# Kernel optimization log

Measured on AMD Instinct MI355X. Metric: run time of the kernel, lower is better.

## Reference

```python
import jax, jax.numpy as jnp
import numpy as np
import math

D_MODEL = 512
N_HEADS = 8
K_NEIGHBORS = 30
B, S = 4, 2048
N_VARIATES = 8
EPS = 1e-5


def layer_norm(x, g, b):
    m = jnp.mean(x, axis=-1, keepdims=True)
    v = jnp.mean(jnp.square(x - m), axis=-1, keepdims=True)
    return (x - m) * jax.lax.rsqrt(v + EPS) * g + b


def mha(x, mask, w_in, b_in, w_out, b_out):
    # x: [B,S,D]; mask: [B,S,S] bool, True = blocked (same for every head)
    Bb, Ss, D = x.shape
    H, dh = N_HEADS, D // N_HEADS
    qkv = x @ w_in.T + b_in                      # [B,S,3D]
    q, k, v = jnp.split(qkv, 3, axis=-1)
    q = q.reshape(Bb, Ss, H, dh).transpose(0, 2, 1, 3)
    k = k.reshape(Bb, Ss, H, dh).transpose(0, 2, 1, 3)
    v = v.reshape(Bb, Ss, H, dh).transpose(0, 2, 1, 3)
    scores = jnp.einsum('bhqd,bhkd->bhqk', q, k) / math.sqrt(dh)
    scores = jnp.where(mask[:, None, :, :], -jnp.inf, scores)
    attn = jax.nn.softmax(scores, axis=-1)
    o = jnp.einsum('bhqk,bhkd->bhqd', attn, v)
    o = o.transpose(0, 2, 1, 3).reshape(Bb, Ss, D)
    return o @ w_out.T + b_out


def build_masks(variates, times, valid_mask):
    Bb, Ss = variates.shape
    eye = jnp.eye(Ss, dtype=bool)
    same_var = variates[:, :, None] == variates[:, None, :]      # [B,S,S]
    valid_2d = valid_mask[:, :, None] & valid_mask[:, None, :]
    intra_mask = ~(same_var & valid_2d)                          # True = blocked
    blocked_i = jnp.any(jnp.all(intra_mask, axis=-1))
    intra_mask = intra_mask & ~(blocked_i & eye)                 # unblock diagonal if any row fully blocked

    diff_var = ~same_var
    time_dist = jnp.abs(times[:, :, None] - times[:, None, :])
    time_dist = jnp.where(~valid_2d | ~diff_var, jnp.inf, time_dist)
    k = min(K_NEIGHBORS, Ss)
    _, topk_idx = jax.lax.top_k(-time_dist, k)                   # k smallest distances
    b_idx = jnp.arange(Bb)[:, None, None]
    r_idx = jnp.arange(Ss)[None, :, None]
    knn_mask = jnp.zeros((Bb, Ss, Ss), dtype=bool).at[b_idx, r_idx, topk_idx].set(True)
    knn_mask = knn_mask & valid_2d
    inter_mask = ~knn_mask
    blocked_e = jnp.any(jnp.all(inter_mask, axis=-1))
    inter_mask = inter_mask & ~(blocked_e & eye)
    return intra_mask, inter_mask


def setup_inputs() -> dict:
    key = jax.random.key(0)
    ks = jax.random.split(key, 12)
    D = D_MODEL
    s = 0.02
    inp = {
        'x': jax.random.normal(ks[0], (B, S, D), dtype=jnp.float32),
        'variates': jax.random.randint(ks[1], (B, S), 0, N_VARIATES),
        'times': jax.random.uniform(ks[2], (B, S), dtype=jnp.float32),
        'valid_mask': jnp.ones((B, S), dtype=bool),
        'in_w1': jax.random.normal(ks[3], (3 * D, D), dtype=jnp.float32) * s,
        'in_b1': jnp.zeros((3 * D,), dtype=jnp.float32),
        'out_w1': jax.random.normal(ks[4], (D, D), dtype=jnp.float32) * s,
        'out_b1': jnp.zeros((D,), dtype=jnp.float32),
        'ln_g1': jnp.ones((D,), dtype=jnp.float32),
        'ln_b1': jnp.zeros((D,), dtype=jnp.float32),
        'in_w2': jax.random.normal(ks[5], (3 * D, D), dtype=jnp.float32) * s,
        'in_b2': jnp.zeros((3 * D,), dtype=jnp.float32),
        'out_w2': jax.random.normal(ks[6], (D, D), dtype=jnp.float32) * s,
        'out_b2': jnp.zeros((D,), dtype=jnp.float32),
        'ln_g2': jnp.ones((D,), dtype=jnp.float32),
        'ln_b2': jnp.zeros((D,), dtype=jnp.float32),
    }
    return inp


def reference(x, variates, times, valid_mask,
              in_w1, in_b1, out_w1, out_b1, ln_g1, ln_b1,
              in_w2, in_b2, out_w2, out_b2, ln_g2, ln_b2):
    intra_mask, inter_mask = build_masks(variates, times, valid_mask)
    a1 = mha(x, intra_mask, in_w1, in_b1, out_w1, out_b1)
    x = layer_norm(x + a1, ln_g1, ln_b1)
    a2 = mha(x, inter_mask, in_w2, in_b2, out_w2, out_b2)
    x = layer_norm(x + a2, ln_g2, ln_b2)
    return x
```

## Files before the change

### kernel.cpp

```cpp
#include <hip/hip_runtime.h>


#define S_LEN 2048
#define BATCH 4
#define DM    512
#define NH    8
#define DH    64
#define KNN_K 30
#define NVAR  8
#define NTOK  (BATCH * S_LEN)
#define QKVD  (3 * DM)
#define PADCAP 2560
#define MAXTILE 40

typedef float f32x4 __attribute__((ext_vector_type(4)));
typedef short s16x8 __attribute__((ext_vector_type(8)));
typedef short s16x4 __attribute__((ext_vector_type(4)));

__device__ __forceinline__ float bf2f(short u) {
  return __uint_as_float(((unsigned)(unsigned short)u) << 16);
}
__device__ __forceinline__ short f2bf(float f) {
  unsigned x = __float_as_uint(f);
  return (short)((x + 0x7fffu + ((x >> 16) & 1u)) >> 16);
}

#define C_N0 (NTOK * DM / 4)
#define C_N1 (QKVD * DM / 4)
#define C_N2 (DM * DM / 4)
#define C_B1 (C_N0 + C_N1)
#define C_B2 (C_B1 + C_N2)
#define C_B3 (C_B2 + C_N1)
#define C_B4 (C_B3 + C_N2)
#define PREP_GRID (2 * BATCH + C_B4 / 1024)

__global__ __launch_bounds__(1024) void prep_cast(
    const int* __restrict__ variates, const float* __restrict__ times,
    int* __restrict__ gcnt, int* __restrict__ pgoff, int* __restrict__ porig,
    int* __restrict__ tileV, int* __restrict__ tileQ0, int* __restrict__ ntile,
    float* __restrict__ flistT, int* __restrict__ flistI, int* __restrict__ flenG,
    int* __restrict__ sortI,
    const float* __restrict__ s0, const float* __restrict__ s1,
    const float* __restrict__ s2, const float* __restrict__ s3,
    const float* __restrict__ s4, short* __restrict__ d0,
    short* __restrict__ d1, short* __restrict__ d2,
    short* __restrict__ d3, short* __restrict__ d4) {
  int blk = blockIdx.x;
  int tid = threadIdx.x;

  if (blk < BATCH) {
    int b = blk;
    __shared__ unsigned hcnt[2048];
    __shared__ int boff[2049];
    __shared__ float bt[S_LEN];
    __shared__ int bp2[S_LEN];
    __shared__ unsigned wsum[16];
    __shared__ unsigned woff[16];

    hcnt[tid] = 0; hcnt[tid + 1024] = 0;
    float t0 = times[b * S_LEN + tid];
    float t1 = times[b * S_LEN + tid + 1024];
    int p0 = (variates[b * S_LEN + tid] << 12) | tid;
    int p1 = (variates[b * S_LEN + tid + 1024] << 12) | (tid + 1024);
    int k0 = (int)(t0 * 2048.0f); k0 = k0 < 0 ? 0 : (k0 > 2047 ? 2047 : k0);
    int k1 = (int)(t1 * 2048.0f); k1 = k1 < 0 ? 0 : (k1 > 2047 ? 2047 : k1);
    __syncthreads();
    atomicAdd(&hcnt[k0], 1u);
    atomicAdd(&hcnt[k1], 1u);
    __syncthreads();
    int wv = tid >> 6, lane = tid & 63;
    int base = wv * 128 + lane * 2;
    unsigned c0 = hcnt[base], c1 = hcnt[base + 1];
    unsigned s = c0 + c1;
    unsigned inc = s;
#pragma unroll
    for (int o2 = 1; o2 < 64; o2 <<= 1) {
      unsigned tt = __shfl_up(inc, o2);
      if (lane >= o2) inc += tt;
    }
    if (lane == 63) wsum[wv] = inc;
    __syncthreads();
    if (tid == 0) {
      unsigned a = 0;
      for (int w2 = 0; w2 < 16; ++w2) { woff[w2] = a; a += wsum[w2]; }
    }
    __syncthreads();
    unsigned e0 = woff[wv] + (inc - s);
    unsigned e1 = e0 + c0;
    boff[base] = (int)e0; boff[base + 1] = (int)e1;
    hcnt[base] = e0; hcnt[base + 1] = e1;
    if (tid == 0) boff[2048] = S_LEN;
    __syncthreads();
    unsigned q0 = atomicAdd(&hcnt[k0], 1u);
    bt[q0] = t0; bp2[q0] = p0;
    unsigned q1 = atomicAdd(&hcnt[k1], 1u);
    bt[q1] = t1; bp2[q1] = p1;
    __syncthreads();
#pragma unroll
    for (int bk = 0; bk < 2; ++bk) {
      int k = tid + bk * 1024;
      int s2 = boff[k], e2 = boff[k + 1];
      for (int i = s2 + 1; i < e2; ++i) {
        float tv = bt[i]; int pv = bp2[i];
        int j = i - 1;
        while (j >= s2 && (bt[j] > tv ||
               (bt[j] == tv && (bp2[j] & 0xFFF) > (pv & 0xFFF)))) {
          bt[j + 1] = bt[j]; bp2[j + 1] = bp2[j]; --j;
        }
        bt[j + 1] = tv; bp2[j + 1] = pv;
      }
    }
    __syncthreads();
    for (int i = tid; i < S_LEN; i += 1024)
      sortI[b * S_LEN + i] = bp2[i] & 0xFFF;
    if (wv < NVAR) {
      int lbase = lane * 32;
      int c = 0;
#pragma unroll
      for (int i = 0; i < 32; ++i) c += ((bp2[lbase + i] >> 12) != wv) ? 1 : 0;
      int pc = c;
#pragma unroll
      for (int o2 = 1; o2 < 64; o2 <<= 1) {
        int t2 = __shfl_up(pc, o2);
        if (lane >= o2) pc += t2;
      }
      int pos = pc - c;
      size_t fb = (size_t)(b * NVAR + wv) * S_LEN;
      for (int i = 0; i < 32; ++i) {
        int e = bp2[lbase + i];
        if ((e >> 12) != wv) {
          flistT[fb + pos] = bt[lbase + i];
          flistI[fb + pos] = e & 0xFFF;
          ++pos;
        }
      }
      if (lane == 63) flenG[b * NVAR + wv] = pc;
    }
  } else if (blk < 2 * BATCH) {
    int b = blk - BATCH;
    int t = tid;
    __shared__ int scnt[64][NVAR];
    __shared__ int soff[64][NVAR];
    __shared__ int stot[NVAR], sbase[NVAR];
    for (int p = t; p < PADCAP; p += 1024) porig[b * PADCAP + p] = -1;
    const int* vb = variates + b * S_LEN;
    int c[NVAR] = {0, 0, 0, 0, 0, 0, 0, 0};
    if (t < 64) {
      for (int j = t * 32; j < t * 32 + 32; ++j) {
        int v = vb[j];
#pragma unroll
        for (int u = 0; u < NVAR; ++u) c[u] += (v == u);
      }
#pragma unroll
      for (int u = 0; u < NVAR; ++u) scnt[t][u] = c[u];
    }
    __syncthreads();
    if (t < NVAR) {
      int a = 0;
      for (int u = 0; u < 64; ++u) { soff[u][t] = a; a += scnt[u][t]; }
      stot[t] = a;
    }
    __syncthreads();
    if (t == 0) {
      int a = 0, nt = 0;
      for (int v = 0; v < NVAR; ++v) {
        sbase[v] = a;
        pgoff[b * NVAR + v] = a;
        gcnt[b * NVAR + v] = stot[v];
        int ntv = (stot[v] + 63) >> 6;
        for (int i = 0; i < ntv; ++i) {
          tileV[b * MAXTILE + nt] = v;
          tileQ0[b * MAXTILE + nt] = a + i * 64;
          ++nt;
        }
        a += ntv * 64;
      }
      ntile[b] = nt;
    }
    __syncthreads();
    if (t < 64) {
      int o[NVAR];
#pragma unroll
      for (int u = 0; u < NVAR; ++u) o[u] = sbase[u] + soff[t][u];
      for (int j = t * 32; j < t * 32 + 32; ++j) {
        int v = vb[j];
        int dst = 0;
#pragma unroll
        for (int u = 0; u < NVAR; ++u) dst += (v == u) ? o[u] : 0;
        porig[b * PADCAP + dst] = j;
#pragma unroll
        for (int u = 0; u < NVAR; ++u) o[u] += (v == u);
      }
    }
  } else {
    int i = (blk - 2 * BATCH) * 1024 + tid;
    const float* src; short* dst; int k;
    if (i < C_N0)      { src = s0; dst = d0; k = i; }
    else if (i < C_B1) { src = s1; dst = d1; k = i - C_N0; }
    else if (i < C_B2) { src = s2; dst = d2; k = i - C_B1; }
    else if (i < C_B3) { src = s3; dst = d3; k = i - C_B2; }
    else               { src = s4; dst = d4; k = i - C_B3; }
    float4 v = ((const float4*)src)[k];
    s16x4 o;
    o[0] = f2bf(v.x); o[1] = f2bf(v.y); o[2] = f2bf(v.z); o[3] = f2bf(v.w);
    ((s16x4*)dst)[k] = o;
  }
}

__global__ __launch_bounds__(256) void knn_grp(const float* __restrict__ times,
                                               const int* __restrict__ porig,
                                               const int* __restrict__ pgoff,
                                               const int* __restrict__ gcnt,
                                               const float* __restrict__ flistT,
                                               const int* __restrict__ flistI,
                                               const int* __restrict__ flenG,
                                               int* __restrict__ out) {
  __shared__ float ft[S_LEN];
  __shared__ int fi[S_LEN];
  int tid = threadIdx.x;
  int bv = blockIdx.x >> 3;
  int chunk = blockIdx.x & 7;
  int b = bv >> 3, v = bv & 7;
  int flen = flenG[bv];
  size_t fb = (size_t)bv * S_LEN;
  for (int i = tid; i < flen; i += 256) {
    ft[i] = flistT[fb + i];
    fi[i] = flistI[fb + i];
  }
  __syncthreads();

  int cnt = gcnt[b * NVAR + v];
  int off = pgoff[b * NVAR + v];
  int qi = chunk * 256 + tid;
  if (qi >= cnt) return;
  int j = porig[b * PADCAP + off + qi];
  float tq = times[b * S_LEN + j];

  int lo = 0, hi = flen;
  while (lo < hi) {
    int mid = (lo + hi) >> 1;
    if (ft[mid] < tq) lo = mid + 1; else hi = mid;
  }
  int L = lo - 1, R = lo;

  float dt[KNN_K];
  int ti[KNN_K];
#pragma unroll
  for (int i = 0; i < KNN_K; ++i) {
    float dL = (L >= 0) ? (tq - ft[L]) : __builtin_inff();
    float dR = (R < flen) ? (ft[R] - tq) : __builtin_inff();
    if (dL <= dR) { dt[i] = dL; ti[i] = fi[L]; --L; }
    else          { dt[i] = dR; ti[i] = fi[R]; ++R; }
  }
  float tau = dt[KNN_K - 1];
  int nLess = 0;
#pragma unroll
  for (int i = 0; i < KNN_K; ++i) nLess += (dt[i] < tau) ? 1 : 0;

  int* op = out + ((size_t)b * S_LEN + j) * KNN_K;
#pragma unroll
  for (int i = 0; i < KNN_K; ++i)
    if (i < nLess) op[i] = ti[i];

  int m = KNN_K - nLess;
  int last = -1;
  for (int s = 0; s < m; ++s) {
    int best = 0x7fffffff;
#pragma unroll
    for (int i = 0; i < KNN_K; ++i)
      if (dt[i] == tau && ti[i] > last && ti[i] < best) best = ti[i];
    for (int Lw = L; Lw >= 0; --Lw) {
      float d = tq - ft[Lw];
      if (d > tau) break;
      if (d == tau) {
        int ix = fi[Lw];
        if (ix > last && ix < best) best = ix;
      }
    }
    for (int Rw = R; Rw < flen; ++Rw) {
      float d = ft[Rw] - tq;
      if (d > tau) break;
      if (d == tau) {
        int ix = fi[Rw];
        if (ix > last && ix < best) best = ix;
      }
    }
    op[nLess + s] = best;
    last = best;
  }
}

template <int OUT_BF16>
__global__ __launch_bounds__(256) void gemm_bt(const short* __restrict__ A,
                                               const short* __restrict__ Bm,
                                               const float* __restrict__ bias,
                                               void* __restrict__ Cout,
                                               int M, int N, int K) {
  __shared__ short sA[128 * 40];
  __shared__ short sB[128 * 40];
  int n0 = blockIdx.x * 128, m0 = blockIdx.y * 128;
  int tid = threadIdx.x;
  int lane = tid & 63, wv = tid >> 6;
  int wr = wv >> 1, wc = wv & 1;

  int srow = tid >> 2;
  int scol = (tid & 3) * 8;
  const short* aG = A + (size_t)(m0 + srow) * K + scol;
  const short* bG = Bm + (size_t)(n0 + srow) * K + scol;

  f32x4 acc[4][4] = {};
  int nk = K >> 5;

  s16x8 pa0 = *(const s16x8*)(aG);
  s16x8 pa1 = *(const s16x8*)(aG + (size_t)64 * K);
  s16x8 pb0 = *(const s16x8*)(bG);
  s16x8 pb1 = *(const s16x8*)(bG + (size_t)64 * K);

  for (int kt = 0; kt < nk; ++kt) {
    __syncthreads();
    *(s16x8*)&sA[srow * 40 + scol] = pa0;
    *(s16x8*)&sA[(srow + 64) * 40 + scol] = pa1;
    *(s16x8*)&sB[srow * 40 + scol] = pb0;
    *(s16x8*)&sB[(srow + 64) * 40 + scol] = pb1;
    __syncthreads();
    if (kt + 1 < nk) {
      const short* a2 = aG + (kt + 1) * 32;
      const short* b2 = bG + (kt + 1) * 32;
      pa0 = *(const s16x8*)(a2);
      pa1 = *(const s16x8*)(a2 + (size_t)64 * K);
      pb0 = *(const s16x8*)(b2);
      pb1 = *(const s16x8*)(b2 + (size_t)64 * K);
    }
    int kb = (lane >> 4) * 8;
    int ar = wr * 64 + (lane & 15);
    int br = wc * 64 + (lane & 15);
    s16x8 af[4], bf[4];
#pragma unroll
    for (int m = 0; m < 4; ++m) af[m] = *(const s16x8*)&sA[(ar + m * 16) * 40 + kb];
#pragma unroll
    for (int n = 0; n < 4; ++n) bf[n] = *(const s16x8*)&sB[(br + n * 16) * 40 + kb];
#pragma unroll
    for (int m = 0; m < 4; ++m)
#pragma unroll
      for (int n = 0; n < 4; ++n)
        acc[m][n] = __builtin_amdgcn_mfma_f32_16x16x32_bf16(af[m], bf[n], acc[m][n], 0, 0, 0);
  }

  int crow0 = m0 + wr * 64 + ((lane >> 4) * 4);
  int ccol0 = n0 + wc * 64 + (lane & 15);
#pragma unroll
  for (int n = 0; n < 4; ++n) {
    int col = ccol0 + n * 16;
    float bv = bias ? bias[col] : 0.f;
#pragma unroll
    for (int m = 0; m < 4; ++m) {
#pragma unroll
      for (int j = 0; j < 4; ++j) {
        int row = crow0 + m * 16 + j;
        float val = acc[m][n][j] + bv;
        if (OUT_BF16)
          ((short*)Cout)[(size_t)row * N + col] = f2bf(val);
        else
          ((float*)Cout)[(size_t)row * N + col] = val;
      }
    }
  }
}

__global__ __launch_bounds__(256) void intra_attn(
    const short* __restrict__ qkv, const int* __restrict__ porig,
    const int* __restrict__ tileV, const int* __restrict__ tileQ0,
    const int* __restrict__ ntile, const int* __restrict__ pgoff,
    const int* __restrict__ gcnt, short* __restrict__ o) {
  int b = blockIdx.z, h = blockIdx.y, t = blockIdx.x;
  if (t >= ntile[b]) return;
  int v = tileV[b * MAXTILE + t];
  int q0 = tileQ0[b * MAXTILE + t];
  int k0 = pgoff[b * NVAR + v];
  int L = gcnt[b * NVAR + v];
  int nch = (L + 63) >> 6;

  __shared__ short sQ[2][64][40];
  __shared__ short sK[2][64][40];
  __shared__ short sVT[2][64][40];
  __shared__ short sP[2][64][40];

  int tid = threadIdx.x, lane = tid & 63, w = tid >> 6;
  int colbase = lane & 15;
  int kfrag = (lane >> 4) * 8;
  int r = tid >> 2, cc = (tid & 3) * 16;

  {
    int tok = porig[b * PADCAP + q0 + r];
    if (tok < 0) tok = 0;
    const short* src = qkv + ((size_t)(b * S_LEN + tok)) * QKVD + h * DH + cc;
    s16x8 v0 = *(const s16x8*)src;
    s16x8 v1 = *(const s16x8*)(src + 8);
    int half = cc >> 5, kk = cc & 31;
    *(s16x8*)&sQ[half][r][kk] = v0;
    *(s16x8*)&sQ[half][r][kk + 8] = v1;
  }

  s16x8 pk0, pk1, pv0, pv1;
  {
    int tok = porig[b * PADCAP + k0 + r];
    if (tok < 0) tok = 0;
    size_t rowg = (size_t)(b * S_LEN + tok) * QKVD;
    const short* srcK = qkv + rowg + DM + h * DH + cc;
    pk0 = *(const s16x8*)srcK;
    pk1 = *(const s16x8*)(srcK + 8);
    const short* srcV = qkv + rowg + 2 * DM + h * DH + cc;
    pv0 = *(const s16x8*)srcV;
    pv1 = *(const s16x8*)(srcV + 8);
  }

  __syncthreads();
  s16x8 aQ0 = *(const s16x8*)&sQ[0][w * 16 + colbase][kfrag];
  s16x8 aQ1 = *(const s16x8*)&sQ[1][w * 16 + colbase][kfrag];

  f32x4 accO[4] = {};
  float lrun[4] = {0.f, 0.f, 0.f, 0.f};

  for (int c = 0; c < nch; ++c) {
    __syncthreads();
    {
      int half = cc >> 5, kk = cc & 31;
      *(s16x8*)&sK[half][r][kk] = pk0;
      *(s16x8*)&sK[half][r][kk + 8] = pk1;
      int khalf = r >> 5, kkv = r & 31;
#pragma unroll
      for (int i = 0; i < 8; ++i) {
        int row = cc + i;
        sVT[khalf][row][kkv ^ (((row >> 4) & 3) << 3)] = pv0[i];
      }
#pragma unroll
      for (int i = 0; i < 8; ++i) {
        int row = cc + 8 + i;
        sVT[khalf][row][kkv ^ (((row >> 4) & 3) << 3)] = pv1[i];
      }
    }
    __syncthreads();
    if (c + 1 < nch) {
      int tok = porig[b * PADCAP + k0 + (c + 1) * 64 + r];
      if (tok < 0) tok = 0;
      size_t rowg = (size_t)(b * S_LEN + tok) * QKVD;
      const short* srcK = qkv + rowg + DM + h * DH + cc;
      pk0 = *(const s16x8*)srcK;
      pk1 = *(const s16x8*)(srcK + 8);
      const short* srcV = qkv + rowg + 2 * DM + h * DH + cc;
      pv0 = *(const s16x8*)srcV;
      pv1 = *(const s16x8*)(srcV + 8);
    }

    f32x4 accS[4] = {};
#pragma unroll
    for (int n = 0; n < 4; ++n) {
      s16x8 b0 = *(const s16x8*)&sK[0][n * 16 + colbase][kfrag];
      s16x8 b1 = *(const s16x8*)&sK[1][n * 16 + colbase][kfrag];
      accS[n] = __builtin_amdgcn_mfma_f32_16x16x32_bf16(aQ0, b0, accS[n], 0, 0, 0);
      accS[n] = __builtin_amdgcn_mfma_f32_16x16x32_bf16(aQ1, b1, accS[n], 0, 0, 0);
    }

    float pv[4][4];
#pragma unroll
    for (int j = 0; j < 4; ++j) {
      float rs = 0.f;
#pragma unroll
      for (int n = 0; n < 4; ++n) {
        bool ok = (c * 64 + n * 16 + colbase) < L;
        float p = ok ? __expf(accS[n][j] * 0.125f) : 0.f;
        pv[n][j] = p;
        rs += p;
      }
      lrun[j] += rs;
    }

    int prow = w * 16 + ((lane >> 4) << 2);
#pragma unroll
    for (int n = 0; n < 4; ++n)
#pragma unroll
      for (int j = 0; j < 4; ++j)
        sP[n >> 1][prow + j][colbase + ((n & 1) << 4)] = f2bf(pv[n][j]);

    s16x8 aP0 = *(const s16x8*)&sP[0][w * 16 + colbase][kfrag];
    s16x8 aP1 = *(const s16x8*)&sP[1][w * 16 + colbase][kfrag];
#pragma unroll
    for (int n = 0; n < 4; ++n) {
      int row = n * 16 + colbase;
      int cb = kfrag ^ ((n & 3) << 3);
      s16x8 b0 = *(const s16x8*)&sVT[0][row][cb];
      s16x8 b1 = *(const s16x8*)&sVT[1][row][cb];
      accO[n] = __builtin_amdgcn_mfma_f32_16x16x32_bf16(aP0, b0, accO[n], 0, 0, 0);
      accO[n] = __builtin_amdgcn_mfma_f32_16x16x32_bf16(aP1, b1, accO[n], 0, 0, 0);
    }
  }

#pragma unroll
  for (int j = 0; j < 4; ++j)
    for (int o2 = 8; o2; o2 >>= 1) lrun[j] += __shfl_xor(lrun[j], o2);

#pragma unroll
  for (int j = 0; j < 4; ++j) {
    int prow = w * 16 + (lane >> 4) * 4 + j;
    int orig = porig[b * PADCAP + q0 + prow];
    if (orig >= 0) {
      float inv = 1.f / lrun[j];
      size_t base = ((size_t)(b * S_LEN + orig)) * DM + h * DH;
#pragma unroll
      for (int n = 0; n < 4; ++n)
        o[base + n * 16 + colbase] = f2bf(accO[n][j] * inv);
    }
  }
}

__global__ __launch_bounds__(256) void inter_attn(const short* __restrict__ qkv,
                                                  const int* __restrict__ knn,
                                                  const int* __restrict__ sortI,
                                                  short* __restrict__ o) {
  __shared__ float sS[4][NH][33];
  __shared__ float sP[4][NH][33];
  int tid = threadIdx.x, lane = tid & 63, w = tid >> 6;
  int rank = blockIdx.x * 4 + w;
  int b = rank >> 11;
  int q = sortI[b * S_LEN + (rank & 2047)];
  int bq = b * S_LEN + q;
  int h = lane >> 3;

  int myidx = (lane < KNN_K) ? knn[(size_t)bq * KNN_K + lane] : 0;

  s16x8 q8 = *(const s16x8*)(qkv + (size_t)bq * QKVD + lane * 8);
  float qf[8];
#pragma unroll
  for (int i = 0; i < 8; ++i) qf[i] = bf2f(q8[i]) * 0.125f;

  for (int j = 0; j < KNN_K; ++j) {
    int idx = __shfl(myidx, j);
    s16x8 k8 = *(const s16x8*)(qkv + ((size_t)(b * S_LEN + idx)) * QKVD + DM + lane * 8);
    float acc = 0.f;
#pragma unroll
    for (int i = 0; i < 8; ++i) acc += qf[i] * bf2f(k8[i]);
    acc += __shfl_xor(acc, 1);
    acc += __shfl_xor(acc, 2);
    acc += __shfl_xor(acc, 4);
    if ((lane & 7) == 0) sS[w][h][j] = acc;
  }

  int jsub = lane & 7;
  float sv0 = sS[w][h][jsub];
  float sv1 = sS[w][h][jsub + 8];
  float sv2 = sS[w][h][jsub + 16];
  float sv3 = (jsub < 6) ? sS[w][h][jsub + 24] : -__builtin_inff();
  float m = fmaxf(fmaxf(sv0, sv1), fmaxf(sv2, sv3));
  m = fmaxf(m, __shfl_xor(m, 1));
  m = fmaxf(m, __shfl_xor(m, 2));
  m = fmaxf(m, __shfl_xor(m, 4));
  float p0 = __expf(sv0 - m), p1 = __expf(sv1 - m), p2 = __expf(sv2 - m);
  float p3 = (jsub < 6) ? __expf(sv3 - m) : 0.f;
  sP[w][h][jsub] = p0;
  sP[w][h][jsub + 8] = p1;
  sP[w][h][jsub + 16] = p2;
  sP[w][h][jsub + 24] = p3;
  float l = p0 + p1 + p2 + p3;
  l += __shfl_xor(l, 1);
  l += __shfl_xor(l, 2);
  l += __shfl_xor(l, 4);

  float o8[8] = {};
  for (int j = 0; j < KNN_K; ++j) {
    int idx = __shfl(myidx, j);
    s16x8 v8 = *(const s16x8*)(qkv + ((size_t)(b * S_LEN + idx)) * QKVD + 2 * DM + lane * 8);
    float p = sP[w][h][j];
#pragma unroll
    for (int i = 0; i < 8; ++i) o8[i] += p * bf2f(v8[i]);
  }
  float inv = 1.f / l;
  s16x8 ov;
#pragma unroll
  for (int i = 0; i < 8; ++i) ov[i] = f2bf(o8[i] * inv);
  *(s16x8*)(o + (size_t)bq * DM + lane * 8) = ov;
}

__global__ __launch_bounds__(256) void residual_ln(const float* __restrict__ x,
                                                   const short* __restrict__ a,
                                                   const float* __restrict__ g,
                                                   const float* __restrict__ bta,
                                                   float* __restrict__ yf,
                                                   short* __restrict__ yb) {
  int row = blockIdx.x * 4 + (threadIdx.x >> 6);
  int lane = threadIdx.x & 63;
  const float4* xp = (const float4*)(x + (size_t)row * DM);
  float4 v0 = xp[lane * 2], v1 = xp[lane * 2 + 1];
  s16x8 a8 = *(const s16x8*)(a + (size_t)row * DM + lane * 8);
  float r[8] = {v0.x + bf2f(a8[0]), v0.y + bf2f(a8[1]),
                v0.z + bf2f(a8[2]), v0.w + bf2f(a8[3]),
                v1.x + bf2f(a8[4]), v1.y + bf2f(a8[5]),
                v1.z + bf2f(a8[6]), v1.w + bf2f(a8[7])};
  float s = 0.f;
#pragma unroll
  for (int j = 0; j < 8; ++j) s += r[j];
  for (int o2 = 32; o2; o2 >>= 1) s += __shfl_xor(s, o2);
  float mean = s * (1.f / DM);
  float vs = 0.f;
#pragma unroll
  for (int j = 0; j < 8; ++j) { float d = r[j] - mean; vs += d * d; }
  for (int o2 = 32; o2; o2 >>= 1) vs += __shfl_xor(vs, o2);
  float inv = rsqrtf(vs * (1.f / DM) + 1e-5f);
  const float4* gp = (const float4*)g;
  const float4* bp = (const float4*)bta;
  float4 g0 = gp[lane * 2], g1 = gp[lane * 2 + 1];
  float4 b0 = bp[lane * 2], b1 = bp[lane * 2 + 1];
  float gg[8] = {g0.x, g0.y, g0.z, g0.w, g1.x, g1.y, g1.z, g1.w};
  float bb[8] = {b0.x, b0.y, b0.z, b0.w, b1.x, b1.y, b1.z, b1.w};
  float y[8];
#pragma unroll
  for (int j = 0; j < 8; ++j) y[j] = (r[j] - mean) * inv * gg[j] + bb[j];
  float4 o0 = {y[0], y[1], y[2], y[3]};
  float4 o1 = {y[4], y[5], y[6], y[7]};
  float4* yp = (float4*)(yf + (size_t)row * DM);
  yp[lane * 2] = o0;
  yp[lane * 2 + 1] = o1;
  if (yb) {
    s16x8 ob;
#pragma unroll
    for (int j = 0; j < 8; ++j) ob[j] = f2bf(y[j]);
    *(s16x8*)(yb + (size_t)row * DM + lane * 8) = ob;
  }
}

extern "C" void kernel_launch(void* const* d_in, const int* in_sizes, int n_in,
                              void* d_out, int out_size, void* d_ws, size_t ws_size,
                              hipStream_t stream) {
  const float* x      = (const float*)d_in[0];
  const int*   var    = (const int*)d_in[1];
  const float* times  = (const float*)d_in[2];
  const float* in_w1  = (const float*)d_in[4];
  const float* in_b1  = (const float*)d_in[5];
  const float* out_w1 = (const float*)d_in[6];
  const float* out_b1 = (const float*)d_in[7];
  const float* ln_g1  = (const float*)d_in[8];
  const float* ln_b1  = (const float*)d_in[9];
  const float* in_w2  = (const float*)d_in[10];
  const float* in_b2  = (const float*)d_in[11];
  const float* out_w2 = (const float*)d_in[12];
  const float* out_b2 = (const float*)d_in[13];
  const float* ln_g2  = (const float*)d_in[14];
  const float* ln_b2  = (const float*)d_in[15];
  float* out = (float*)d_out;

  char* ws = (char*)d_ws;
  size_t off = 0;
  auto alloc = [&](size_t bytes) -> char* {
    char* p = ws + off;
    off = (off + bytes + 255) & ~(size_t)255;
    return p;
  };
  short* xb    = (short*)alloc((size_t)NTOK * DM * 2);
  short* x1b   = (short*)alloc((size_t)NTOK * DM * 2);
  short* w1q   = (short*)alloc((size_t)QKVD * DM * 2);
  short* w1o   = (short*)alloc((size_t)DM * DM * 2);
  short* w2q   = (short*)alloc((size_t)QKVD * DM * 2);
  short* w2o   = (short*)alloc((size_t)DM * DM * 2);
  short* qkvb  = (short*)alloc((size_t)NTOK * QKVD * 2);
  short* ob    = (short*)alloc((size_t)NTOK * DM * 2);
  short* afb   = (short*)alloc((size_t)NTOK * DM * 2);
  float* x1f   = (float*)alloc((size_t)NTOK * DM * 4);
  int* gcnt    = (int*)alloc((size_t)BATCH * NVAR * 4);
  int* pgoff   = (int*)alloc((size_t)BATCH * NVAR * 4);
  int* porig   = (int*)alloc((size_t)BATCH * PADCAP * 4);
  int* tileV   = (int*)alloc((size_t)BATCH * MAXTILE * 4);
  int* tileQ0  = (int*)alloc((size_t)BATCH * MAXTILE * 4);
  int* ntile   = (int*)alloc((size_t)BATCH * 4);
  int* knn     = (int*)alloc((size_t)NTOK * KNN_K * 4);
  float* flistT = (float*)alloc((size_t)BATCH * NVAR * S_LEN * 4);
  int*   flistI = (int*)alloc((size_t)BATCH * NVAR * S_LEN * 4);
  int*   flenG  = (int*)alloc((size_t)BATCH * NVAR * 4);
  int*   sortI  = (int*)alloc((size_t)NTOK * 4);

  prep_cast<<<PREP_GRID, 1024, 0, stream>>>(
      var, times, gcnt, pgoff, porig, tileV, tileQ0, ntile,
      flistT, flistI, flenG, sortI,
      x, in_w1, out_w1, in_w2, out_w2, xb, w1q, w1o, w2q, w2o);

  knn_grp<<<BATCH * NVAR * 8, 256, 0, stream>>>(times, porig, pgoff, gcnt,
                                                flistT, flistI, flenG, knn);

  gemm_bt<1><<<dim3(QKVD / 128, NTOK / 128), 256, 0, stream>>>(xb, w1q, in_b1, qkvb,
                                                               NTOK, QKVD, DM);
  intra_attn<<<dim3(MAXTILE, NH, BATCH), 256, 0, stream>>>(qkvb, porig, tileV, tileQ0,
                                                           ntile, pgoff, gcnt, ob);
  gemm_bt<1><<<dim3(DM / 128, NTOK / 128), 256, 0, stream>>>(ob, w1o, out_b1, afb,
                                                             NTOK, DM, DM);
  residual_ln<<<NTOK / 4, 256, 0, stream>>>(x, afb, ln_g1, ln_b1, x1f, x1b);

  gemm_bt<1><<<dim3(QKVD / 128, NTOK / 128), 256, 0, stream>>>(x1b, w2q, in_b2, qkvb,
                                                               NTOK, QKVD, DM);
  inter_attn<<<NTOK / 4, 256, 0, stream>>>(qkvb, knn, sortI, ob);
  gemm_bt<1><<<dim3(DM / 128, NTOK / 128), 256, 0, stream>>>(ob, w2o, out_b2, afb,
                                                             NTOK, DM, DM);
  residual_ln<<<NTOK / 4, 256, 0, stream>>>(x1f, afb, ln_g2, ln_b2, out, nullptr);
}
```

Baseline: 189.5 us.

## Fuse kNN search and first QKV GEMM into one launch via block-index split

```diff
diff --git a/kernel.cpp b/kernel.cpp
--- a/kernel.cpp
+++ b/kernel.cpp
@@ -12,6 +12,8 @@
 #define QKVD  (3 * DM)
 #define PADCAP 2560
 #define MAXTILE 40
+#define KNN_BLKS (BATCH * NVAR * 8)
+#define G1_NB    ((QKVD / 128) * (NTOK / 128))
 
 typedef float f32x4 __attribute__((ext_vector_type(4)));
 typedef short s16x8 __attribute__((ext_vector_type(8)));
@@ -207,86 +209,158 @@
   }
 }
 
-__global__ __launch_bounds__(256) void knn_grp(const float* __restrict__ times,
-                                               const int* __restrict__ porig,
-                                               const int* __restrict__ pgoff,
-                                               const int* __restrict__ gcnt,
-                                               const float* __restrict__ flistT,
-                                               const int* __restrict__ flistI,
-                                               const int* __restrict__ flenG,
-                                               int* __restrict__ out) {
-  __shared__ float ft[S_LEN];
-  __shared__ int fi[S_LEN];
+__global__ __launch_bounds__(256) void knn_gemm1(
+    const float* __restrict__ times, const int* __restrict__ porig,
+    const int* __restrict__ pgoff, const int* __restrict__ gcnt,
+    const float* __restrict__ flistT, const int* __restrict__ flistI,
+    const int* __restrict__ flenG, int* __restrict__ knnout,
+    const short* __restrict__ A, const short* __restrict__ Bm,
+    const float* __restrict__ bias, short* __restrict__ Cout) {
+  __shared__ char smem[20480];
+  int blk = blockIdx.x;
   int tid = threadIdx.x;
-  int bv = blockIdx.x >> 3;
-  int chunk = blockIdx.x & 7;
-  int b = bv >> 3, v = bv & 7;
-  int flen = flenG[bv];
-  size_t fb = (size_t)bv * S_LEN;
-  for (int i = tid; i < flen; i += 256) {
-    ft[i] = flistT[fb + i];
-    fi[i] = flistI[fb + i];
-  }
-  __syncthreads();
-
-  int cnt = gcnt[b * NVAR + v];
-  int off = pgoff[b * NVAR + v];
-  int qi = chunk * 256 + tid;
-  if (qi >= cnt) return;
-  int j = porig[b * PADCAP + off + qi];
-  float tq = times[b * S_LEN + j];
-
-  int lo = 0, hi = flen;
-  while (lo < hi) {
-    int mid = (lo + hi) >> 1;
-    if (ft[mid] < tq) lo = mid + 1; else hi = mid;
-  }
-  int L = lo - 1, R = lo;
-
-  float dt[KNN_K];
-  int ti[KNN_K];
-#pragma unroll
-  for (int i = 0; i < KNN_K; ++i) {
-    float dL = (L >= 0) ? (tq - ft[L]) : __builtin_inff();
-    float dR = (R < flen) ? (ft[R] - tq) : __builtin_inff();
-    if (dL <= dR) { dt[i] = dL; ti[i] = fi[L]; --L; }
-    else          { dt[i] = dR; ti[i] = fi[R]; ++R; }
-  }
-  float tau = dt[KNN_K - 1];
-  int nLess = 0;
-#pragma unroll
-  for (int i = 0; i < KNN_K; ++i) nLess += (dt[i] < tau) ? 1 : 0;
-
-  int* op = out + ((size_t)b * S_LEN + j) * KNN_K;
-#pragma unroll
-  for (int i = 0; i < KNN_K; ++i)
-    if (i < nLess) op[i] = ti[i];
-
-  int m = KNN_K - nLess;
-  int last = -1;
-  for (int s = 0; s < m; ++s) {
-    int best = 0x7fffffff;
+
+  if (blk < KNN_BLKS) {
+    float* ft = (float*)smem;
+    int* fi = (int*)(smem + 8192);
+    int bv = blk >> 3;
+    int chunk = blk & 7;
+    int b = bv >> 3, v = bv & 7;
+    int flen = flenG[bv];
+    size_t fb = (size_t)bv * S_LEN;
+    for (int i = tid; i < flen; i += 256) {
+      ft[i] = flistT[fb + i];
+      fi[i] = flistI[fb + i];
+    }
+    __syncthreads();
+
+    int cnt = gcnt[b * NVAR + v];
+    int off = pgoff[b * NVAR + v];
+    int qi = chunk * 256 + tid;
+    if (qi >= cnt) return;
+    int j = porig[b * PADCAP + off + qi];
+    float tq = times[b * S_LEN + j];
+
+    int lo = 0, hi = flen;
+    while (lo < hi) {
+      int mid = (lo + hi) >> 1;
+      if (ft[mid] < tq) lo = mid + 1; else hi = mid;
+    }
+    int L = lo - 1, R = lo;
+
+    float dt[KNN_K];
+    int ti[KNN_K];
+#pragma unroll
+    for (int i = 0; i < KNN_K; ++i) {
+      float dL = (L >= 0) ? (tq - ft[L]) : __builtin_inff();
+      float dR = (R < flen) ? (ft[R] - tq) : __builtin_inff();
+      if (dL <= dR) { dt[i] = dL; ti[i] = fi[L]; --L; }
+      else          { dt[i] = dR; ti[i] = fi[R]; ++R; }
+    }
+    float tau = dt[KNN_K - 1];
+    int nLess = 0;
+#pragma unroll
+    for (int i = 0; i < KNN_K; ++i) nLess += (dt[i] < tau) ? 1 : 0;
+
+    int* op = knnout + ((size_t)b * S_LEN + j) * KNN_K;
 #pragma unroll
     for (int i = 0; i < KNN_K; ++i)
-      if (dt[i] == tau && ti[i] > last && ti[i] < best) best = ti[i];
-    for (int Lw = L; Lw >= 0; --Lw) {
-      float d = tq - ft[Lw];
-      if (d > tau) break;
-      if (d == tau) {
-        int ix = fi[Lw];
-        if (ix > last && ix < best) best = ix;
-      }
-    }
-    for (int Rw = R; Rw < flen; ++Rw) {
-      float d = ft[Rw] - tq;
-      if (d > tau) break;
-      if (d == tau) {
-        int ix = fi[Rw];
-        if (ix > last && ix < best) best = ix;
-      }
-    }
-    op[nLess + s] = best;
-    last = best;
+      if (i < nLess) op[i] = ti[i];
+
+    int m = KNN_K - nLess;
+    int last = -1;
+    for (int s = 0; s < m; ++s) {
+      int best = 0x7fffffff;
+#pragma unroll
+      for (int i = 0; i < KNN_K; ++i)
+        if (dt[i] == tau && ti[i] > last && ti[i] < best) best = ti[i];
+      for (int Lw = L; Lw >= 0; --Lw) {
+        float d = tq - ft[Lw];
+        if (d > tau) break;
+        if (d == tau) {
+          int ix = fi[Lw];
+          if (ix > last && ix < best) best = ix;
+        }
+      }
+      for (int Rw = R; Rw < flen; ++Rw) {
+        float d = ft[Rw] - tq;
+        if (d > tau) break;
+        if (d == tau) {
+          int ix = fi[Rw];
+          if (ix > last && ix < best) best = ix;
+        }
+      }
+      op[nLess + s] = best;
+      last = best;
+    }
+  } else {
+    short* sA = (short*)smem;
+    short* sB = (short*)(smem + 10240);
+    int blk2 = blk - KNN_BLKS;
+    int n0 = (blk2 % (QKVD / 128)) * 128;
+    int m0 = (blk2 / (QKVD / 128)) * 128;
+    const int K = DM, N = QKVD;
+    int lane = tid & 63, wv = tid >> 6;
+    int wr = wv >> 1, wc = wv & 1;
+
+    int srow = tid >> 2;
+    int scol = (tid & 3) * 8;
+    const short* aG = A + (size_t)(m0 + srow) * K + scol;
+    const short* bG = Bm + (size_t)(n0 + srow) * K + scol;
+
+    f32x4 acc[4][4] = {};
+    int nk = K >> 5;
+
+    s16x8 pa0 = *(const s16x8*)(aG);
+    s16x8 pa1 = *(const s16x8*)(aG + (size_t)64 * K);
+    s16x8 pb0 = *(const s16x8*)(bG);
+    s16x8 pb1 = *(const s16x8*)(bG + (size_t)64 * K);
+
+    for (int kt = 0; kt < nk; ++kt) {
+      __syncthreads();
+      *(s16x8*)&sA[srow * 40 + scol] = pa0;
+      *(s16x8*)&sA[(srow + 64) * 40 + scol] = pa1;
+      *(s16x8*)&sB[srow * 40 + scol] = pb0;
+      *(s16x8*)&sB[(srow + 64) * 40 + scol] = pb1;
+      __syncthreads();
+      if (kt + 1 < nk) {
+        const short* a2 = aG + (kt + 1) * 32;
+        const short* b2 = bG + (kt + 1) * 32;
+        pa0 = *(const s16x8*)(a2);
+        pa1 = *(const s16x8*)(a2 + (size_t)64 * K);
+        pb0 = *(const s16x8*)(b2);
+        pb1 = *(const s16x8*)(b2 + (size_t)64 * K);
+      }
+      int kb = (lane >> 4) * 8;
+      int ar = wr * 64 + (lane & 15);
+      int br = wc * 64 + (lane & 15);
+      s16x8 af[4], bf[4];
+#pragma unroll
+      for (int m = 0; m < 4; ++m) af[m] = *(const s16x8*)&sA[(ar + m * 16) * 40 + kb];
+#pragma unroll
+      for (int n = 0; n < 4; ++n) bf[n] = *(const s16x8*)&sB[(br + n * 16) * 40 + kb];
+#pragma unroll
+      for (int m = 0; m < 4; ++m)
+#pragma unroll
+        for (int n = 0; n < 4; ++n)
+          acc[m][n] = __builtin_amdgcn_mfma_f32_16x16x32_bf16(af[m], bf[n], acc[m][n], 0, 0, 0);
+    }
+
+    int crow0 = m0 + wr * 64 + ((lane >> 4) * 4);
+    int ccol0 = n0 + wc * 64 + (lane & 15);
+#pragma unroll
+    for (int n = 0; n < 4; ++n) {
+      int col = ccol0 + n * 16;
+      float bv = bias[col];
+#pragma unroll
+      for (int m = 0; m < 4; ++m) {
+#pragma unroll
+        for (int j = 0; j < 4; ++j) {
+          int row = crow0 + m * 16 + j;
+          Cout[(size_t)row * N + col] = f2bf(acc[m][n][j] + bv);
+        }
+      }
+    }
   }
 }
 
@@ -681,11 +755,10 @@
       flistT, flistI, flenG, sortI,
       x, in_w1, out_w1, in_w2, out_w2, xb, w1q, w1o, w2q, w2o);
 
-  knn_grp<<<BATCH * NVAR * 8, 256, 0, stream>>>(times, porig, pgoff, gcnt,
-                                                flistT, flistI, flenG, knn);
-
-  gemm_bt<1><<<dim3(QKVD / 128, NTOK / 128), 256, 0, stream>>>(xb, w1q, in_b1, qkvb,
-                                                               NTOK, QKVD, DM);
+  knn_gemm1<<<KNN_BLKS + G1_NB, 256, 0, stream>>>(
+      times, porig, pgoff, gcnt, flistT, flistI, flenG, knn,
+      xb, w1q, in_b1, qkvb);
+
   intra_attn<<<dim3(MAXTILE, NH, BATCH), 256, 0, stream>>>(qkvb, porig, tileV, tileQ0,
                                                            ntile, pgoff, gcnt, ob);
   gemm_bt<1><<<dim3(DM / 128, NTOK / 128), 256, 0, stream>>>(ob, w1o, out_b1, afb,
```

After: 182.8 us, median of 2. 3.5% less time.
